# Optimization experiments

Measured on AMD Instinct MI355X. Metric: run time of the kernel, lower is better.

## Reference

```python
import jax, jax.numpy as jnp
import numpy as np

B, N, D_MODEL, H, LIN_K = 4, 4096, 1024, 16, 256
D_K = D_MODEL // H


def setup_inputs() -> dict:
    key = jax.random.key(0)
    ks = jax.random.split(key, 9)
    s = 1.0 / np.sqrt(D_MODEL)
    return {
        "K": jax.random.normal(ks[0], (B, N, D_MODEL), jnp.float32),
        "Q": jax.random.normal(ks[1], (B, N, D_MODEL), jnp.float32),
        "V": jax.random.normal(ks[2], (B, N, D_MODEL), jnp.float32),
        "We": jax.random.normal(ks[3], (N, LIN_K), jnp.float32) / np.sqrt(N),
        "be": jnp.zeros((LIN_K,), jnp.float32),
        "Wf": jax.random.normal(ks[4], (N, LIN_K), jnp.float32) / np.sqrt(N),
        "bf": jnp.zeros((LIN_K,), jnp.float32),
        "Wo": jax.random.normal(ks[5], (D_MODEL, D_MODEL), jnp.float32) * s,
        "bo": jnp.zeros((D_MODEL,), jnp.float32),
        "n_heads": H,
    }


def reference(K, Q, V, We, be, Wf, bf, Wo, bo, n_heads):
    b, n, d_model = K.shape
    d_k = d_model // n_heads
    split = lambda x: x.reshape(b, n, n_heads, d_k).transpose(0, 2, 1, 3)  # [b,h,n,d]
    Kh, Qh, Vh = split(K), split(Q), split(V)
    # Linformer projection: Dense(k) applied to K^T [b,h,d,n] -> [b,h,d,k]
    Kp = jnp.einsum("bhnd,nk->bhdk", Kh, We) + be
    scores = jnp.einsum("bhnd,bhdk->bhnk", Qh, Kp) / jnp.sqrt(jnp.float32(d_k))
    P = jax.nn.softmax(scores, axis=-1)  # dropout rate 0.0 -> identity
    # V projection: Dense(k) on V^T then transpose back -> [b,h,k,d]
    Vp = jnp.einsum("bhnd,nk->bhkd", Vh, Wf) + bf[:, None]
    out = jnp.einsum("bhnk,bhkd->bhnd", P, Vp)
    out = out.transpose(0, 2, 1, 3).reshape(b, n, d_model)
    return out @ Wo + bo
```

## Files before the change

kernel.cpp:

```cpp
#include <hip/hip_runtime.h>
#include <hip/hip_bf16.h>

#define BB      4
#define SEQ     4096
#define DMODEL  1024
#define NHEAD   16
#define DK      64
#define LK      256
#define BH      (BB*NHEAD)

typedef unsigned short u16;
typedef unsigned int   u32;
typedef float f32x4  __attribute__((ext_vector_type(4)));
typedef _Float16 f16x8 __attribute__((ext_vector_type(8)));

__device__ __forceinline__ u16 f2h(float f) {
    _Float16 h = (_Float16)f;
    u16 r; __builtin_memcpy(&r, &h, 2); return r;
}
__device__ __forceinline__ u32 packh(float a, float b) {
    return (u32)f2h(a) | ((u32)f2h(b) << 16);
}
__device__ __forceinline__ f16x8 pack8h(float4 a, float4 b) {
    union { uint4 u; f16x8 h; } r;
    r.u = make_uint4(packh(a.x, a.y), packh(a.z, a.w),
                     packh(b.x, b.y), packh(b.z, b.w));
    return r.h;
}
__device__ __forceinline__ void gl2lds16(const void* g, void* l) {
    __builtin_amdgcn_global_load_lds(
        (const __attribute__((address_space(1))) unsigned int*)g,
        (__attribute__((address_space(3))) unsigned int*)l,
        16, 0, 0);
}

__global__ __launch_bounds__(256) void tconv(
    const float* __restrict__ src, u16* __restrict__ dst,
    int ss, int ds, size_t sbo, size_t dbo)
{
    const float* S = src + (size_t)blockIdx.z * sbo;
    u16* D         = dst + (size_t)blockIdx.z * dbo;
    const int r0 = blockIdx.x * 64;
    const int c0 = blockIdx.y * 64;
    __shared__ float T[64][65];
    const int t = threadIdx.x;
    {
        int rr = (t >> 4) * 4;
        int cc = (t & 15) * 4;
#pragma unroll
        for (int i = 0; i < 4; ++i) {
            float4 v = *(const float4*)(S + (size_t)(r0 + rr + i) * ss + c0 + cc);
            T[rr + i][cc + 0] = v.x; T[rr + i][cc + 1] = v.y;
            T[rr + i][cc + 2] = v.z; T[rr + i][cc + 3] = v.w;
        }
    }
    __syncthreads();
    int cr = t >> 2, rc = (t & 3) * 16;
    u32 o[8];
#pragma unroll
    for (int j = 0; j < 8; ++j)
        o[j] = packh(T[rc + 2 * j][cr], T[rc + 2 * j + 1][cr]);
    u16* d = D + (size_t)(c0 + cr) * ds + r0 + rc;
    *(uint4*)(d)     = make_uint4(o[0], o[1], o[2], o[3]);
    *(uint4*)(d + 8) = make_uint4(o[4], o[5], o[6], o[7]);
}

__global__ __launch_bounds__(256) void wo_convert(
    const float* __restrict__ Wo, u16* __restrict__ WoT)
{
    const int n0 = blockIdx.x * 64, k0 = blockIdx.y * 64;
    __shared__ float T[64][65];
    const int t = threadIdx.x;
    {
        int kr = (t >> 4) * 4;
        int nc = (t & 15) * 4;
#pragma unroll
        for (int i = 0; i < 4; ++i) {
            float4 v = *(const float4*)(Wo + (size_t)(k0 + kr + i) * DMODEL + n0 + nc);
            T[kr + i][nc + 0] = v.x; T[kr + i][nc + 1] = v.y;
            T[kr + i][nc + 2] = v.z; T[kr + i][nc + 3] = v.w;
        }
    }
    __syncthreads();
    int n = t >> 2, kc = (t & 3) * 16;
    u32 o[8];
#pragma unroll
    for (int j = 0; j < 8; ++j)
        o[j] = packh(T[kc + j * 2][n], T[kc + j * 2 + 1][n]);
    u16* dst = WoT + (size_t)(n0 + n) * DMODEL + k0 + kc;
    *(uint4*)(dst)     = make_uint4(o[0], o[1], o[2], o[3]);
    *(uint4*)(dst + 8) = make_uint4(o[4], o[5], o[6], o[7]);
}

#define PROJ_BODY(Ab, Bb, bias, Cb, bias_on_row, c_row_stride, c0, r0)          \
    const int t  = threadIdx.x;                                                 \
    const int lane = t & 63;                                                    \
    const int w  = t >> 6;                                                      \
    const int wr = w >> 1, wc = w & 1;                                          \
    const int q  = lane >> 4, c = lane & 15;                                    \
    __shared__ u16 As[2][128 * 64];                                             \
    __shared__ u16 Bs[2][128 * 64];                                             \
    auto stage = [&](int buf, int kk) {                                         \
        _Pragma("unroll")                                                       \
        for (int i = 0; i < 4; ++i) {                                           \
            int li  = i * 256 + t;                                              \
            int row = li >> 3;                                                  \
            int c8  = (li & 7) ^ (row & 7);                                     \
            gl2lds16(Ab + (size_t)(r0 + row) * SEQ + kk + c8 * 8, &As[buf][(size_t)li * 8]); \
            gl2lds16(Bb + (size_t)(c0 + row) * SEQ + kk + c8 * 8, &Bs[buf][(size_t)li * 8]); \
        }                                                                       \
    };                                                                          \
    f32x4 acc[4][4];                                                            \
    _Pragma("unroll")                                                           \
    for (int m = 0; m < 4; ++m)                                                 \
        _Pragma("unroll")                                                       \
        for (int n = 0; n < 4; ++n) acc[m][n] = (f32x4){0.f, 0.f, 0.f, 0.f};    \
    stage(0, 0);                                                                \
    __syncthreads();                                                            \
    int cur = 0;                                                                \
    for (int k0 = 0; k0 < SEQ; k0 += 64) {                                      \
        if (k0 + 64 < SEQ) stage(cur ^ 1, k0 + 64);                             \
        _Pragma("unroll")                                                       \
        for (int s = 0; s < 2; ++s) {                                           \
            f16x8 af[4], bf[4];                                                 \
            _Pragma("unroll")                                                   \
            for (int m = 0; m < 4; ++m) {                                       \
                int row = wr * 64 + m * 16 + c;                                 \
                int c8  = (s * 4 + q) ^ (row & 7);                              \
                af[m] = *(const f16x8*)&As[cur][row * 64 + c8 * 8];             \
            }                                                                   \
            _Pragma("unroll")                                                   \
            for (int n = 0; n < 4; ++n) {                                       \
                int row = wc * 64 + n * 16 + c;                                 \
                int c8  = (s * 4 + q) ^ (row & 7);                              \
                bf[n] = *(const f16x8*)&Bs[cur][row * 64 + c8 * 8];             \
            }                                                                   \
            _Pragma("unroll")                                                   \
            for (int m = 0; m < 4; ++m)                                         \
                _Pragma("unroll")                                               \
                for (int n = 0; n < 4; ++n)                                     \
                    acc[m][n] = __builtin_amdgcn_mfma_f32_16x16x32_f16(af[m], bf[n], acc[m][n], 0, 0, 0); \
        }                                                                       \
        __syncthreads();                                                        \
        cur ^= 1;                                                               \
    }                                                                           \
    if (bias_on_row) {                                                          \
        _Pragma("unroll")                                                       \
        for (int m = 0; m < 4; ++m) {                                           \
            int rowb = r0 + wr * 64 + m * 16 + q * 4;                           \
            _Pragma("unroll")                                                   \
            for (int r = 0; r < 4; ++r) {                                       \
                float bv = bias[rowb + r];                                      \
                u16* dst = Cb + (size_t)(rowb + r) * c_row_stride + c0 + wc * 64 + c; \
                _Pragma("unroll")                                               \
                for (int n = 0; n < 4; ++n) dst[n * 16] = f2h(acc[m][n][r] + bv); \
            }                                                                   \
        }                                                                       \
    } else {                                                                    \
        float bv[4];                                                            \
        _Pragma("unroll")                                                       \
        for (int n = 0; n < 4; ++n) bv[n] = bias[c0 + wc * 64 + n * 16 + c];    \
        _Pragma("unroll")                                                       \
        for (int m = 0; m < 4; ++m) {                                           \
            int rowb = r0 + wr * 64 + m * 16 + q * 4;                           \
            _Pragma("unroll")                                                   \
            for (int r = 0; r < 4; ++r) {                                       \
                u16* dst = Cb + (size_t)(rowb + r) * c_row_stride + c0 + wc * 64 + c; \
                _Pragma("unroll")                                               \
                for (int n = 0; n < 4; ++n) dst[n * 16] = f2h(acc[m][n][r] + bv[n]); \
            }                                                                   \
        }                                                                       \
    }

__global__ __launch_bounds__(256) void proj_gemm(
    const u16* __restrict__ A, const u16* __restrict__ B,
    const float* __restrict__ bias, u16* __restrict__ Cout,
    int bias_on_row, size_t a_batch, size_t b_batch,
    int c_row_stride, size_t c_batch)
{
    const u16* Ab = A + (size_t)blockIdx.z * a_batch;
    const u16* Bb = B + (size_t)blockIdx.z * b_batch;
    u16* Cb       = Cout + (size_t)blockIdx.z * c_batch;
    const int c0 = blockIdx.x * 128;
    const int r0 = blockIdx.y * 128;
    PROJ_BODY(Ab, Bb, bias, Cb, bias_on_row, c_row_stride, c0, r0)
}

__global__ __launch_bounds__(256) void proj_both(
    const u16* __restrict__ WeT, const u16* __restrict__ WfT,
    const u16* __restrict__ KT,  const u16* __restrict__ VT,
    const float* __restrict__ be, const float* __restrict__ bfp,
    u16* __restrict__ KpF, u16* __restrict__ VpF)
{
    const int id = blockIdx.x;
    const u16 *Ab, *Bb; const float* bias; u16* Cb;
    int bias_on_row, c_row_stride, c0, r0;
    if (id < 64) {
        int b = id >> 4, s = id & 15;
        c0 = (s & 7) * 128; r0 = (s >> 3) * 128;
        Ab = WeT; Bb = KT + (size_t)b * DMODEL * SEQ;
        bias = be; bias_on_row = 1;
        Cb = KpF + (size_t)b * LK * DMODEL; c_row_stride = DMODEL;
    } else {
        int j = id - 64, b = j >> 4, s = j & 15;
        c0 = (s & 1) * 128; r0 = (s >> 1) * 128;
        Ab = VT + (size_t)b * DMODEL * SEQ; Bb = WfT;
        bias = bfp; bias_on_row = 0;
        Cb = VpF + (size_t)b * DMODEL * LK; c_row_stride = LK;
    }
    PROJ_BODY(Ab, Bb, bias, Cb, bias_on_row, c_row_stride, c0, r0)
}

__global__ __launch_bounds__(512) void attn_mfma(
    const float* __restrict__ Qin, const u16* __restrict__ KpF,
    const u16* __restrict__ VpF,   u16* __restrict__ AO)
{
    const int bh = blockIdx.y, b = bh >> 4, h = bh & 15;
    const int n0 = blockIdx.x * 1024;
    const int t  = threadIdx.x;
    const int w    = t >> 6;
    const int lane = t & 63;
    const int q    = lane >> 4;
    const int c    = lane & 15;

    __shared__ u16 Kl[16384];
    __shared__ u16 Vl[16384];
    __shared__ u16 Pl[128 * 264];

    const u16* kbase = KpF + (size_t)b * LK * DMODEL + h * DK;
#pragma unroll
    for (int i = 0; i < 4; ++i) {
        int li = i * 512 + t;
        int row = li >> 3, ch = li & 7;
        int chs = ch ^ (row & 7);
        gl2lds16(kbase + (size_t)row * DMODEL + chs * 8, Kl + (size_t)li * 8);
    }
    const u16* vbase = VpF + ((size_t)b * DMODEL + h * DK) * LK;
#pragma unroll
    for (int i = 0; i < 4; ++i) {
        int li = i * 512 + t;
        int row = li >> 5, ch = li & 31;
        int chs = (ch & 24) | ((ch & 7) ^ (row & 7));
        gl2lds16(vbase + (size_t)row * LK + chs * 8, Vl + (size_t)li * 8);
    }
    __syncthreads();

    const float* qbase = Qin + ((size_t)b * SEQ + n0 + w * 16 + c) * DMODEL + h * DK;
    const float4* qp0 = (const float4*)qbase;
    float4 q0 = qp0[2 * q], q1 = qp0[2 * q + 1];
    float4 q2 = qp0[8 + 2 * q], q3 = qp0[8 + 2 * q + 1];

    for (int p = 0; p < 8; ++p) {
        f16x8 a0 = pack8h(q0, q1);
        f16x8 a1 = pack8h(q2, q3);
        if (p < 7) {
            const float4* qp = (const float4*)(qbase + (size_t)(p + 1) * 128 * DMODEL);
            q0 = qp[2 * q]; q1 = qp[2 * q + 1];
            q2 = qp[8 + 2 * q]; q3 = qp[8 + 2 * q + 1];
        }

        f32x4 sc[16];
#pragma unroll
        for (int nt = 0; nt < 16; ++nt) sc[nt] = (f32x4){0.f, 0.f, 0.f, 0.f};
#pragma unroll
        for (int nt = 0; nt < 16; ++nt) {
            int ra = (nt * 16 + c) * 64;
            f16x8 b0 = *(const f16x8*)&Kl[ra + ((q ^ (c & 7)) * 8)];
            f16x8 b1 = *(const f16x8*)&Kl[ra + (((4 + q) ^ (c & 7)) * 8)];
            sc[nt] = __builtin_amdgcn_mfma_f32_16x16x32_f16(a0, b0, sc[nt], 0, 0, 0);
            sc[nt] = __builtin_amdgcn_mfma_f32_16x16x32_f16(a1, b1, sc[nt], 0, 0, 0);
        }

        float mx[4] = {-1e30f, -1e30f, -1e30f, -1e30f};
#pragma unroll
        for (int nt = 0; nt < 16; ++nt) {
            sc[nt] *= 0.125f;
#pragma unroll
            for (int r = 0; r < 4; ++r) mx[r] = fmaxf(mx[r], sc[nt][r]);
        }
#pragma unroll
        for (int d = 1; d < 16; d <<= 1)
#pragma unroll
            for (int r = 0; r < 4; ++r) mx[r] = fmaxf(mx[r], __shfl_xor(mx[r], d, 64));

        float sm[4] = {0.f, 0.f, 0.f, 0.f};
#pragma unroll
        for (int nt = 0; nt < 16; ++nt)
#pragma unroll
            for (int r = 0; r < 4; ++r) {
                float e = __expf(sc[nt][r] - mx[r]);
                sc[nt][r] = e;
                sm[r] += e;
            }
#pragma unroll
        for (int d = 1; d < 16; d <<= 1)
#pragma unroll
            for (int r = 0; r < 4; ++r) sm[r] += __shfl_xor(sm[r], d, 64);
        float inv[4];
#pragma unroll
        for (int r = 0; r < 4; ++r) inv[r] = 1.0f / sm[r];

#pragma unroll
        for (int nt = 0; nt < 16; ++nt)
#pragma unroll
            for (int r = 0; r < 4; ++r)
                Pl[(w * 16 + q * 4 + r) * 264 + nt * 16 + c] = f2h(sc[nt][r] * inv[r]);

        f32x4 ov[4];
#pragma unroll
        for (int nt = 0; nt < 4; ++nt) ov[nt] = (f32x4){0.f, 0.f, 0.f, 0.f};
#pragma unroll
        for (int ks = 0; ks < 8; ++ks) {
            f16x8 pa = *(const f16x8*)&Pl[(w * 16 + c) * 264 + ks * 32 + q * 8];
#pragma unroll
            for (int nt = 0; nt < 4; ++nt) {
                int chunk = ks * 4 + q;
                int chs = (chunk & 24) | ((chunk & 7) ^ (c & 7));
                f16x8 vf = *(const f16x8*)&Vl[(nt * 16 + c) * 256 + chs * 8];
                ov[nt] = __builtin_amdgcn_mfma_f32_16x16x32_f16(pa, vf, ov[nt], 0, 0, 0);
            }
        }

#pragma unroll
        for (int nt = 0; nt < 4; ++nt)
#pragma unroll
            for (int r = 0; r < 4; ++r)
                Pl[(w * 16 + q * 4 + r) * 264 + nt * 16 + c] = f2h(ov[nt][r]);

#pragma unroll
        for (int ps = 0; ps < 2; ++ps) {
            int lr  = w * 16 + ps * 8 + (lane >> 3);
            int col = (lane & 7) * 8;
            uint4 vv = *(uint4*)&Pl[lr * 264 + col];
            *(uint4*)(AO + ((size_t)b * SEQ + n0 + p * 128 + lr) * DMODEL + h * DK + col) = vv;
        }
    }
}

#define OBM 128
#define OBN 128
#define OBK 64

__global__ __launch_bounds__(256) void out_gemm_mfma(
    const u16* __restrict__ AO, const u16* __restrict__ WoT,
    const float* __restrict__ bo, float* __restrict__ Out)
{
    const int c0 = blockIdx.x * OBN;
    const int r0 = blockIdx.y * OBM;
    const int t  = threadIdx.x;
    const int lane = t & 63;
    const int w  = t >> 6;
    const int wr = w >> 1, wc = w & 1;
    const int q  = lane >> 4, c = lane & 15;

    __shared__ u16 As[OBM * OBK];
    __shared__ u16 Bs[OBN * OBK];

    f32x4 acc[4][4];
#pragma unroll
    for (int m = 0; m < 4; ++m)
#pragma unroll
        for (int n = 0; n < 4; ++n) acc[m][n] = (f32x4){0.f, 0.f, 0.f, 0.f};

    for (int k0 = 0; k0 < DMODEL; k0 += OBK) {
#pragma unroll
        for (int i = 0; i < 4; ++i) {
            int li  = i * 256 + t;
            int row = li >> 3;
            int c8  = (li & 7) ^ (row & 7);
            gl2lds16(AO  + (size_t)(r0 + row) * DMODEL + k0 + c8 * 8, (u16*)As + (size_t)li * 8);
            gl2lds16(WoT + (size_t)(c0 + row) * DMODEL + k0 + c8 * 8, (u16*)Bs + (size_t)li * 8);
        }
        __syncthreads();

#pragma unroll
        for (int s = 0; s < 2; ++s) {
            f16x8 af[4], bf[4];
#pragma unroll
            for (int m = 0; m < 4; ++m) {
                int row = wr * 64 + m * 16 + c;
                int c8  = (s * 4 + q) ^ (row & 7);
                af[m] = *(const f16x8*)&As[row * 64 + c8 * 8];
            }
#pragma unroll
            for (int n = 0; n < 4; ++n) {
                int row = wc * 64 + n * 16 + c;
                int c8  = (s * 4 + q) ^ (row & 7);
                bf[n] = *(const f16x8*)&Bs[row * 64 + c8 * 8];
            }
#pragma unroll
            for (int m = 0; m < 4; ++m)
#pragma unroll
                for (int n = 0; n < 4; ++n)
                    acc[m][n] = __builtin_amdgcn_mfma_f32_16x16x32_f16(af[m], bf[n], acc[m][n], 0, 0, 0);
        }
        __syncthreads();
    }

    float bv[4];
#pragma unroll
    for (int n = 0; n < 4; ++n) bv[n] = bo[c0 + wc * 64 + n * 16 + c];
#pragma unroll
    for (int m = 0; m < 4; ++m) {
        int rowb = r0 + wr * 64 + m * 16 + q * 4;
#pragma unroll
        for (int r = 0; r < 4; ++r) {
            float* dst = Out + (size_t)(rowb + r) * DMODEL + c0 + wc * 64 + c;
#pragma unroll
            for (int n = 0; n < 4; ++n) dst[n * 16] = acc[m][n][r] + bv[n];
        }
    }
}

extern "C" void kernel_launch(void* const* d_in, const int* in_sizes, int n_in,
                              void* d_out, int out_size, void* d_ws, size_t ws_size,
                              hipStream_t stream)
{
    const float* K   = (const float*)d_in[0];
    const float* Q   = (const float*)d_in[1];
    const float* V   = (const float*)d_in[2];
    const float* We  = (const float*)d_in[3];
    const float* be  = (const float*)d_in[4];
    const float* Wf  = (const float*)d_in[5];
    const float* bfp = (const float*)d_in[6];
    const float* Wo  = (const float*)d_in[7];
    const float* bo  = (const float*)d_in[8];
    float* Out = (float*)d_out;

    const size_t M1 = 1048576;
    const size_t TB = (size_t)BB * DMODEL * SEQ;

    if (ws_size >= 2 * (4 * M1 + 2 * TB)) {
        u16* KpF = (u16*)d_ws;
        u16* VpF = KpF + M1;
        u16* WeT = VpF + M1;
        u16* WfT = WeT + M1;
        u16* KT  = WfT + M1;
        u16* VT  = KT + TB;
        u16* AO  = KT;
        u16* WoT = WeT;

        tconv<<<dim3(SEQ / 64, LK / 64, 1), 256, 0, stream>>>(We, WeT, LK, SEQ, 0, 0);
        tconv<<<dim3(SEQ / 64, LK / 64, 1), 256, 0, stream>>>(Wf, WfT, LK, SEQ, 0, 0);
        tconv<<<dim3(SEQ / 64, DMODEL / 64, BB), 256, 0, stream>>>(
            K, KT, DMODEL, SEQ, (size_t)SEQ * DMODEL, (size_t)DMODEL * SEQ);
        tconv<<<dim3(SEQ / 64, DMODEL / 64, BB), 256, 0, stream>>>(
            V, VT, DMODEL, SEQ, (size_t)SEQ * DMODEL, (size_t)DMODEL * SEQ);
        proj_both<<<dim3(128), 256, 0, stream>>>(WeT, WfT, KT, VT, be, bfp, KpF, VpF);
        wo_convert<<<dim3(DMODEL / 64, DMODEL / 64), 256, 0, stream>>>(Wo, WoT);
        attn_mfma<<<dim3(4, BH), 512, 0, stream>>>(Q, KpF, VpF, AO);
        out_gemm_mfma<<<dim3(DMODEL / OBN, (BB * SEQ) / OBM), 256, 0, stream>>>(AO, WoT, bo, Out);
    } else {
        u16* KpF = (u16*)d_ws;
        u16* VpF = KpF + (size_t)BB * LK * DMODEL;
        u16* BIG = VpF + (size_t)BB * DMODEL * LK;
        u16* Wsm = BIG + (size_t)BB * SEQ * DMODEL;

        tconv<<<dim3(SEQ / 64, LK / 64, 1), 256, 0, stream>>>(We, Wsm, LK, SEQ, 0, 0);
        tconv<<<dim3(SEQ / 64, DMODEL / 64, BB), 256, 0, stream>>>(
            K, BIG, DMODEL, SEQ, (size_t)SEQ * DMODEL, (size_t)DMODEL * SEQ);
        proj_gemm<<<dim3(DMODEL / 128, LK / 128, BB), 256, 0, stream>>>(
            Wsm, BIG, be, KpF, 1, (size_t)0, (size_t)DMODEL * SEQ, DMODEL, (size_t)LK * DMODEL);
        tconv<<<dim3(SEQ / 64, LK / 64, 1), 256, 0, stream>>>(Wf, Wsm, LK, SEQ, 0, 0);
        tconv<<<dim3(SEQ / 64, DMODEL / 64, BB), 256, 0, stream>>>(
            V, BIG, DMODEL, SEQ, (size_t)SEQ * DMODEL, (size_t)DMODEL * SEQ);
        proj_gemm<<<dim3(LK / 128, DMODEL / 128, BB), 256, 0, stream>>>(
            BIG, Wsm, bfp, VpF, 0, (size_t)DMODEL * SEQ, (size_t)0, LK, (size_t)DMODEL * LK);
        wo_convert<<<dim3(DMODEL / 64, DMODEL / 64), 256, 0, stream>>>(Wo, Wsm);
        attn_mfma<<<dim3(4, BH), 512, 0, stream>>>(Q, KpF, VpF, BIG);
        out_gemm_mfma<<<dim3(DMODEL / OBN, (BB * SEQ) / OBM), 256, 0, stream>>>(BIG, Wsm, bo, Out);
    }
}
```

Baseline: 379.6 us.

## Split-K projection GEMMs, merge transpose launches, and remap block order for locality

Merges the separate transpose/convert launches (We, Wf, K, V, Wo) into one tconv_all kernel. The Linformer projection GEMMs are split along the sequence dimension into 4 parts (512 blocks instead of 128) to fill the GPU, with a new reduce kernel that sums the fp32 partials, adds bias and converts to fp16. Attention and output GEMM blocks are remapped with an XCD-aware swizzle so neighbouring tiles share L2. This costs extra workspace and extra fp32 partial traffic, and falls back to the old path if workspace is too small.

```diff
diff --git a/kernel.cpp b/kernel.cpp
--- a/kernel.cpp
+++ b/kernel.cpp
@@ -8,6 +8,7 @@
 #define DK      64
 #define LK      256
 #define BH      (BB*NHEAD)
+#define SPLITK  4
 
 typedef unsigned short u16;
 typedef unsigned int   u32;
@@ -34,16 +35,11 @@
         16, 0, 0);
 }
 
-__global__ __launch_bounds__(256) void tconv(
-    const float* __restrict__ src, u16* __restrict__ dst,
-    int ss, int ds, size_t sbo, size_t dbo)
-{
-    const float* S = src + (size_t)blockIdx.z * sbo;
-    u16* D         = dst + (size_t)blockIdx.z * dbo;
-    const int r0 = blockIdx.x * 64;
-    const int c0 = blockIdx.y * 64;
+__device__ __forceinline__ void tconv_body(
+    const float* __restrict__ S, u16* __restrict__ D,
+    int ss, int ds, int r0, int c0, int t)
+{
     __shared__ float T[64][65];
-    const int t = threadIdx.x;
     {
         int rr = (t >> 4) * 4;
         int cc = (t & 15) * 4;
@@ -65,31 +61,49 @@
     *(uint4*)(d + 8) = make_uint4(o[4], o[5], o[6], o[7]);
 }
 
+__global__ __launch_bounds__(256) void tconv(
+    const float* __restrict__ src, u16* __restrict__ dst,
+    int ss, int ds, size_t sbo, size_t dbo)
+{
+    tconv_body(src + (size_t)blockIdx.z * sbo, dst + (size_t)blockIdx.z * dbo,
+               ss, ds, blockIdx.x * 64, blockIdx.y * 64, threadIdx.x);
+}
+
 __global__ __launch_bounds__(256) void wo_convert(
     const float* __restrict__ Wo, u16* __restrict__ WoT)
 {
-    const int n0 = blockIdx.x * 64, k0 = blockIdx.y * 64;
-    __shared__ float T[64][65];
-    const int t = threadIdx.x;
-    {
-        int kr = (t >> 4) * 4;
-        int nc = (t & 15) * 4;
-#pragma unroll
-        for (int i = 0; i < 4; ++i) {
-            float4 v = *(const float4*)(Wo + (size_t)(k0 + kr + i) * DMODEL + n0 + nc);
-            T[kr + i][nc + 0] = v.x; T[kr + i][nc + 1] = v.y;
-            T[kr + i][nc + 2] = v.z; T[kr + i][nc + 3] = v.w;
-        }
-    }
-    __syncthreads();
-    int n = t >> 2, kc = (t & 3) * 16;
-    u32 o[8];
-#pragma unroll
-    for (int j = 0; j < 8; ++j)
-        o[j] = packh(T[kc + j * 2][n], T[kc + j * 2 + 1][n]);
-    u16* dst = WoT + (size_t)(n0 + n) * DMODEL + k0 + kc;
-    *(uint4*)(dst)     = make_uint4(o[0], o[1], o[2], o[3]);
-    *(uint4*)(dst + 8) = make_uint4(o[4], o[5], o[6], o[7]);
+    tconv_body(Wo, WoT, DMODEL, DMODEL, blockIdx.y * 64, blockIdx.x * 64, threadIdx.x);
+}
+
+__global__ __launch_bounds__(256) void tconv_all(
+    const float* __restrict__ We, const float* __restrict__ Wf,
+    const float* __restrict__ K,  const float* __restrict__ V,
+    const float* __restrict__ Wo,
+    u16* __restrict__ WeT, u16* __restrict__ WfT,
+    u16* __restrict__ KT,  u16* __restrict__ VT, u16* __restrict__ WoT)
+{
+    const int id = blockIdx.x;
+    const float* S; u16* D; int ss, ds, r0, c0;
+    if (id < 512) {
+        int j = id & 255;
+        S  = (id < 256) ? We : Wf;
+        D  = (id < 256) ? WeT : WfT;
+        ss = LK; ds = SEQ;
+        r0 = (j & 63) * 64; c0 = (j >> 6) * 64;
+    } else if (id < 8704) {
+        int j  = id - 512;
+        int isV = j >= 4096; if (isV) j -= 4096;
+        int bz = j >> 10, rem = j & 1023;
+        S  = (isV ? V : K) + (size_t)bz * SEQ * DMODEL;
+        D  = (isV ? VT : KT) + (size_t)bz * DMODEL * SEQ;
+        ss = DMODEL; ds = SEQ;
+        r0 = (rem & 63) * 64; c0 = (rem >> 6) * 64;
+    } else {
+        int j = id - 8704;
+        S = Wo; D = WoT; ss = DMODEL; ds = DMODEL;
+        r0 = (j & 15) * 64; c0 = (j >> 4) * 64;
+    }
+    tconv_body(S, D, ss, ds, r0, c0, threadIdx.x);
 }
 
 #define PROJ_BODY(Ab, Bb, bias, Cb, bias_on_row, c_row_stride, c0, r0)          \
@@ -211,12 +225,127 @@
     PROJ_BODY(Ab, Bb, bias, Cb, bias_on_row, c_row_stride, c0, r0)
 }
 
+__global__ __launch_bounds__(256) void proj_split(
+    const u16* __restrict__ WeT, const u16* __restrict__ WfT,
+    const u16* __restrict__ KT,  const u16* __restrict__ VT,
+    float* __restrict__ PPK, float* __restrict__ PPV)
+{
+    const int sk = blockIdx.x >> 7;
+    const int id = blockIdx.x & 127;
+    const u16 *Ab, *Bb; float* Pout;
+    int crs, c0, r0;
+    if (id < 64) {
+        int b = id >> 4, s = id & 15;
+        c0 = (s & 7) * 128; r0 = (s >> 3) * 128;
+        Ab = WeT; Bb = KT + (size_t)b * DMODEL * SEQ;
+        Pout = PPK + ((size_t)sk * BB + b) * (LK * DMODEL); crs = DMODEL;
+    } else {
+        int j = id - 64, b = j >> 4, s = j & 15;
+        c0 = (s & 1) * 128; r0 = (s >> 1) * 128;
+        Ab = VT + (size_t)b * DMODEL * SEQ; Bb = WfT;
+        Pout = PPV + ((size_t)sk * BB + b) * (DMODEL * LK); crs = LK;
+    }
+    const int kbeg = sk * (SEQ / SPLITK), kend = kbeg + SEQ / SPLITK;
+
+    const int t  = threadIdx.x;
+    const int lane = t & 63;
+    const int w  = t >> 6;
+    const int wr = w >> 1, wc = w & 1;
+    const int q  = lane >> 4, c = lane & 15;
+    __shared__ u16 As[2][128 * 64];
+    __shared__ u16 Bs[2][128 * 64];
+    auto stage = [&](int buf, int kk) {
+#pragma unroll
+        for (int i = 0; i < 4; ++i) {
+            int li  = i * 256 + t;
+            int row = li >> 3;
+            int c8  = (li & 7) ^ (row & 7);
+            gl2lds16(Ab + (size_t)(r0 + row) * SEQ + kk + c8 * 8, &As[buf][(size_t)li * 8]);
+            gl2lds16(Bb + (size_t)(c0 + row) * SEQ + kk + c8 * 8, &Bs[buf][(size_t)li * 8]);
+        }
+    };
+    f32x4 acc[4][4];
+#pragma unroll
+    for (int m = 0; m < 4; ++m)
+#pragma unroll
+        for (int n = 0; n < 4; ++n) acc[m][n] = (f32x4){0.f, 0.f, 0.f, 0.f};
+    stage(0, kbeg);
+    __syncthreads();
+    int cur = 0;
+    for (int k0 = kbeg; k0 < kend; k0 += 64) {
+        if (k0 + 64 < kend) stage(cur ^ 1, k0 + 64);
+#pragma unroll
+        for (int s = 0; s < 2; ++s) {
+            f16x8 af[4], bf[4];
+#pragma unroll
+            for (int m = 0; m < 4; ++m) {
+                int row = wr * 64 + m * 16 + c;
+                int c8  = (s * 4 + q) ^ (row & 7);
+                af[m] = *(const f16x8*)&As[cur][row * 64 + c8 * 8];
+            }
+#pragma unroll
+            for (int n = 0; n < 4; ++n) {
+                int row = wc * 64 + n * 16 + c;
+                int c8  = (s * 4 + q) ^ (row & 7);
+                bf[n] = *(const f16x8*)&Bs[cur][row * 64 + c8 * 8];
+            }
+#pragma unroll
+            for (int m = 0; m < 4; ++m)
+#pragma unroll
+                for (int n = 0; n < 4; ++n)
+                    acc[m][n] = __builtin_amdgcn_mfma_f32_16x16x32_f16(af[m], bf[n], acc[m][n], 0, 0, 0);
+        }
+        __syncthreads();
+        cur ^= 1;
+    }
+#pragma unroll
+    for (int m = 0; m < 4; ++m) {
+        int rowb = r0 + wr * 64 + m * 16 + q * 4;
+#pragma unroll
+        for (int r = 0; r < 4; ++r) {
+            float* dst = Pout + (size_t)(rowb + r) * crs + c0 + wc * 64 + c;
+#pragma unroll
+            for (int n = 0; n < 4; ++n) dst[n * 16] = acc[m][n][r];
+        }
+    }
+}
+
+__global__ __launch_bounds__(256) void proj_reduce(
+    const float* __restrict__ PPK, const float* __restrict__ PPV,
+    const float* __restrict__ be,  const float* __restrict__ bfp,
+    u16* __restrict__ KpF, u16* __restrict__ VpF)
+{
+    const int isV = blockIdx.y;
+    const float* P    = isV ? PPV : PPK;
+    const float* bias = isV ? bfp : be;
+    u16* Out          = isV ? VpF : KpF;
+    const size_t flat = ((size_t)blockIdx.x * 256 + threadIdx.x) * 4;
+    const size_t skstride = (size_t)BB * LK * DMODEL;
+    float4 a = *(const float4*)(P + flat);
+#pragma unroll
+    for (int sk = 1; sk < SPLITK; ++sk) {
+        float4 p = *(const float4*)(P + (size_t)sk * skstride + flat);
+        a.x += p.x; a.y += p.y; a.z += p.z; a.w += p.w;
+    }
+    if (!isV) {
+        float bv = bias[(flat >> 10) & 255];
+        a.x += bv; a.y += bv; a.z += bv; a.w += bv;
+    } else {
+        float4 bv = *(const float4*)(bias + (flat & 255));
+        a.x += bv.x; a.y += bv.y; a.z += bv.z; a.w += bv.w;
+    }
+    uint2 o = make_uint2(packh(a.x, a.y), packh(a.z, a.w));
+    *(uint2*)(Out + flat) = o;
+}
+
 __global__ __launch_bounds__(512) void attn_mfma(
     const float* __restrict__ Qin, const u16* __restrict__ KpF,
     const u16* __restrict__ VpF,   u16* __restrict__ AO)
 {
-    const int bh = blockIdx.y, b = bh >> 4, h = bh & 15;
-    const int n0 = blockIdx.x * 1024;
+    const int lin = blockIdx.x + blockIdx.y * gridDim.x;
+    const int tid = (lin & 7) * 32 + (lin >> 3);
+    const int bh = tid >> 2, b = bh >> 4, h = bh & 15;
+    const int n0 = (tid & 3) * 1024;
     const int t  = threadIdx.x;
     const int w    = t >> 6;
     const int lane = t & 63;
@@ -345,8 +474,10 @@
     const u16* __restrict__ AO, const u16* __restrict__ WoT,
     const float* __restrict__ bo, float* __restrict__ Out)
 {
-    const int c0 = blockIdx.x * OBN;
-    const int r0 = blockIdx.y * OBM;
+    const int lin = blockIdx.x + blockIdx.y * gridDim.x;
+    const int tid = (lin & 7) * 128 + (lin >> 3);
+    const int r0 = (tid >> 3) * OBM;
+    const int c0 = (tid & 7) * OBN;
     const int t  = threadIdx.x;
     const int lane = t & 63;
     const int w  = t >> 6;
@@ -429,8 +560,28 @@
 
     const size_t M1 = 1048576;
     const size_t TB = (size_t)BB * DMODEL * SEQ;
-
-    if (ws_size >= 2 * (4 * M1 + 2 * TB)) {
+    const size_t PFLOATS = (size_t)SPLITK * BB * LK * DMODEL;
+    const size_t NEED_SPLIT = (5 * M1 + 2 * TB) * 2 + 2 * PFLOATS * 4;
+    const size_t NEED_PAR   = 2 * (4 * M1 + 2 * TB);
+
+    if (ws_size >= NEED_SPLIT) {
+        u16* KpF = (u16*)d_ws;
+        u16* VpF = KpF + M1;
+        u16* WeT = VpF + M1;
+        u16* WfT = WeT + M1;
+        u16* WoT = WfT + M1;
+        u16* KT  = WoT + M1;
+        u16* VT  = KT + TB;
+        float* PPK = (float*)(VT + TB);
+        float* PPV = PPK + PFLOATS;
+        u16* AO  = KT;
+
+        tconv_all<<<dim3(8960), 256, 0, stream>>>(We, Wf, K, V, Wo, WeT, WfT, KT, VT, WoT);
+        proj_split<<<dim3(128 * SPLITK), 256, 0, stream>>>(WeT, WfT, KT, VT, PPK, PPV);
+        proj_reduce<<<dim3(1024, 2), 256, 0, stream>>>(PPK, PPV, be, bfp, KpF, VpF);
+        attn_mfma<<<dim3(4, BH), 512, 0, stream>>>(Q, KpF, VpF, AO);
+        out_gemm_mfma<<<dim3(DMODEL / OBN, (BB * SEQ) / OBM), 256, 0, stream>>>(AO, WoT, bo, Out);
+    } else if (ws_size >= NEED_PAR) {
         u16* KpF = (u16*)d_ws;
         u16* VpF = KpF + M1;
         u16* WeT = VpF + M1;
```

After: 337.5 us. -11.1%, faster.
